# Kernel optimization log

Hardware: AMD Instinct MI355X
Metric: run time of the kernel (lower is better)

The kernel has to match this reference:

```python
import jax, jax.numpy as jnp
import numpy as np

ASPECT = 1.0
SCALE = 0.3
MIN_PATCH_H = 60.0
EPS = 1e-6


def _make_patch_boxes(boxes, H, W):
    # Patcher.create: per detected box, compute [ymin_patch, xmin_patch, patch_h, patch_w]
    ymin, xmin, ymax, xmax = jnp.split(boxes, 4, axis=-1)
    h = ymax - ymin
    w = xmax - xmin
    pw = h * SCALE
    ph = ASPECT * pw
    oy = ymin + h / 2.0
    ox = xmin + w / 2.0
    yp = jnp.maximum(oy - ph / 2.0, 0.0)
    xp = jnp.maximum(ox - pw / 2.0, 0.0)
    yp = jnp.where(yp + ph > H, H - ph, yp)
    xp = jnp.where(xp + pw > W, W - pw, xp)
    return jnp.concatenate([yp, xp, ph, pw], axis=-1)  # [B, N, 4]


def _bilinear(src, rel_y, rel_x, out_h, out_w):
    # tf.image.resize bilinear (half-pixel centers): sample src [P,P,3] at the
    # grid of an (out_h, out_w) resize, evaluated at all H/W image offsets.
    P = src.shape[0]
    sy = jnp.clip((rel_y + 0.5) * P / out_h - 0.5, 0.0, P - 1.0)  # [H]
    sx = jnp.clip((rel_x + 0.5) * P / out_w - 0.5, 0.0, P - 1.0)  # [W]
    y0 = jnp.floor(sy).astype(jnp.int32); y1 = jnp.minimum(y0 + 1, P - 1)
    x0 = jnp.floor(sx).astype(jnp.int32); x1 = jnp.minimum(x0 + 1, P - 1)
    wy = (sy - y0.astype(sy.dtype))[:, None, None]
    wx = (sx - x0.astype(sx.dtype))[None, :, None]
    top = (1.0 - wx) * src[y0[:, None], x0[None, :]] + wx * src[y0[:, None], x1[None, :]]
    bot = (1.0 - wx) * src[y1[:, None], x0[None, :]] + wx * src[y1[:, None], x1[None, :]]
    return (1.0 - wy) * top + wy * bot  # [H, W, 3]


def _forward(images, boxes, patch):
    B, H, W, _ = images.shape
    pboxes = _make_patch_boxes(boxes, float(H), float(W))  # [B, N, 4]
    valid = pboxes[..., 2] > MIN_PATCH_H                    # gather_nd filter
    p_mean = patch.mean((0, 1))
    p_std = patch.std((0, 1)) + EPS
    ys = jnp.arange(H, dtype=jnp.int32)
    xs = jnp.arange(W, dtype=jnp.int32)

    def per_image(image, pbs, vls):
        # serial while_loop over patches: later patches overwrite earlier ones,
        # and histogram match uses the current (already-patched) background.
        def step(img, bv):
            pb, v = bv
            pbi = pb.astype(jnp.int32)  # tf.cast truncation
            y0, x0, ph, pw = pbi[0], pbi[1], pbi[2], pbi[3]
            in_y = (ys >= y0) & (ys < y0 + ph)
            in_x = (xs >= x0) & (xs < x0 + pw)
            mask = in_y[:, None] & in_x[None, :]            # [H, W]
            mf = mask[..., None].astype(img.dtype)
            cnt = jnp.maximum(mask.sum().astype(img.dtype), 1.0)
            bg_mean = (img * mf).sum((0, 1)) / cnt
            bg_std = jnp.sqrt((((img - bg_mean) ** 2) * mf).sum((0, 1)) / cnt) + EPS
            # histogram match (per-channel moment matching) of patch to background
            matched = (patch - p_mean) / p_std * bg_std + bg_mean
            phf = jnp.maximum(ph.astype(img.dtype), 1.0)
            pwf = jnp.maximum(pw.astype(img.dtype), 1.0)
            sampled = _bilinear(matched,
                                (ys - y0).astype(img.dtype),
                                (xs - x0).astype(img.dtype), phf, pwf)
            img = jnp.where(mask[..., None] & v, sampled, img)
            return img, None

        img, _ = jax.lax.scan(step, image, (pbs, vls))
        return img

    return jax.vmap(per_image)(images, pboxes, valid)


def setup_inputs() -> dict:
    key = jax.random.key(0)
    k1, k2, k3 = jax.random.split(key, 3)
    B, N, H, W, P = 16, 16, 512, 512, 512
    images = jax.random.normal(k1, (B, H, W, 3), dtype=jnp.float32)
    u = jax.random.uniform(k2, (B, N, 4), dtype=jnp.float32)
    ymin = u[..., 0] * (H - 320)
    xmin = u[..., 1] * (W - 320)
    h = 150.0 + u[..., 2] * 150.0
    w = 150.0 + u[..., 3] * 150.0
    boxes = jnp.stack([ymin, xmin, ymin + h, xmin + w], axis=-1)
    patch = jax.random.normal(k3, (P, P, 3), dtype=jnp.float32) * 0.5
    return {"images": images, "boxes": boxes, "patch": patch}


def reference(images, boxes, patch):
    return _forward(images, boxes, patch)
```

## Files before the change

kernel.cpp:

```cpp
#include <hip/hip_runtime.h>
#include <math.h>

#define IMG_H 512
#define IMG_W 512
#define PSIZE 512
#define NIMG 16
#define NBOX 16
#define RED_BLOCKS 256
#define Z0 4
#define SLOTS 20

#define WS_PMEAN 0
#define WS_PSTD  3
#define WS_PART  6
#define WS_PAIR  1544
#define WS_COEF  (1544 + 256 * SLOTS * 8)

typedef float f4u __attribute__((ext_vector_type(4), aligned(4)));
typedef float f2u __attribute__((ext_vector_type(2), aligned(4)));

struct BoxGeo { int y0, x0, ph, pw, valid; };

__device__ __forceinline__ BoxGeo make_geo(const float* bx) {
    float ymin = bx[0], xmin = bx[1], ymax = bx[2], xmax = bx[3];
    float h = ymax - ymin, w = xmax - xmin;
    float pwf = h * 0.3f;
    float phf = 1.0f * pwf;
    float oy = ymin + h * 0.5f;
    float ox = xmin + w * 0.5f;
    float yp = fmaxf(oy - phf * 0.5f, 0.0f);
    float xp = fmaxf(ox - pwf * 0.5f, 0.0f);
    if (yp + phf > (float)IMG_H) yp = (float)IMG_H - phf;
    if (xp + pwf > (float)IMG_W) xp = (float)IMG_W - pwf;
    BoxGeo g;
    g.y0 = (int)yp; g.x0 = (int)xp;
    g.ph = (int)phf; g.pw = (int)pwf;
    g.valid = (phf > 60.0f) ? 1 : 0;
    return g;
}

__device__ __forceinline__ void bsample_fast(const float* __restrict__ patch,
                                             int relY, int relX,
                                             float phf, float pwf, float s[3]) {
    float sy = ((float)relY + 0.5f) * (float)PSIZE / phf - 0.5f;
    sy = fminf(fmaxf(sy, 0.0f), (float)(PSIZE - 1));
    float sx = ((float)relX + 0.5f) * (float)PSIZE / pwf - 0.5f;
    sx = fminf(fmaxf(sx, 0.0f), (float)(PSIZE - 1));
    int y0 = (int)floorf(sy);
    int y1 = min(y0 + 1, PSIZE - 1);
    int x0 = (int)floorf(sx);
    float wy = sy - (float)y0;
    float wx = sx - (float)x0;
    const int baseX = min(x0, PSIZE - 2);
    const bool hi = (x0 == PSIZE - 1);
    const float* r0 = patch + (y0 * PSIZE + baseX) * 3;
    const float* r1 = patch + (y1 * PSIZE + baseX) * 3;
    f4u a0 = *(const f4u*)r0; f2u b0 = *(const f2u*)(r0 + 4);
    f4u a1 = *(const f4u*)r1; f2u b1 = *(const f2u*)(r1 + 4);
    float p00c, p01c, p10c, p11c, top, bot;
    p00c = hi ? a0.w : a0.x;  p01c = a0.w;
    p10c = hi ? a1.w : a1.x;  p11c = a1.w;
    top = (1.f - wx) * p00c + wx * p01c;
    bot = (1.f - wx) * p10c + wx * p11c;
    s[0] = (1.f - wy) * top + wy * bot;
    p00c = hi ? b0.x : a0.y;  p01c = b0.x;
    p10c = hi ? b1.x : a1.y;  p11c = b1.x;
    top = (1.f - wx) * p00c + wx * p01c;
    bot = (1.f - wx) * p10c + wx * p11c;
    s[1] = (1.f - wy) * top + wy * bot;
    p00c = hi ? b0.y : a0.z;  p01c = b0.y;
    p10c = hi ? b1.y : a1.z;  p11c = b1.y;
    top = (1.f - wx) * p00c + wx * p01c;
    bot = (1.f - wx) * p10c + wx * p11c;
    s[2] = (1.f - wy) * top + wy * bot;
}

template<int N, int NWAVES>
__device__ __forceinline__ void block_reduceN(float v[N]) {
    __shared__ float lds[NWAVES][N];
    const int lane = threadIdx.x & 63;
    const int wave = threadIdx.x >> 6;
    __syncthreads();
#pragma unroll
    for (int k = 0; k < N; ++k) {
#pragma unroll
        for (int off = 32; off > 0; off >>= 1)
            v[k] += __shfl_down(v[k], off, 64);
    }
    if (lane == 0) {
#pragma unroll
        for (int k = 0; k < N; ++k) lds[wave][k] = v[k];
    }
    __syncthreads();
    if (wave == 0) {
#pragma unroll
        for (int k = 0; k < N; ++k) {
            float x = (lane < NWAVES) ? lds[lane][k] : 0.0f;
#pragma unroll
            for (int off = 32; off > 0; off >>= 1)
                x += __shfl_down(x, off, 64);
            if (lane == 0) lds[0][k] = x;
        }
    }
    __syncthreads();
#pragma unroll
    for (int k = 0; k < N; ++k) v[k] = lds[0][k];
}

__global__ void patch_stats_partial(const float* __restrict__ patch,
                                    float* __restrict__ ws) {
    const int g = blockIdx.x * 256 + threadIdx.x;
    const float4* p4 = (const float4*)patch;
    float4 a = p4[3 * g], b = p4[3 * g + 1], c = p4[3 * g + 2];
    float v[6];
    v[0] = a.x + a.w + b.z + c.y;
    v[1] = a.y + b.x + b.w + c.z;
    v[2] = a.z + b.y + c.x + c.w;
    v[3] = a.x*a.x + a.w*a.w + b.z*b.z + c.y*c.y;
    v[4] = a.y*a.y + b.x*b.x + b.w*b.w + c.z*c.z;
    v[5] = a.z*a.z + b.y*b.y + c.x*c.x + c.w*c.w;
    block_reduceN<6, 4>(v);
    if (threadIdx.x == 0) {
        float* o = ws + WS_PART + blockIdx.x * 6;
#pragma unroll
        for (int k = 0; k < 6; ++k) o[k] = v[k];
    }
}

__global__ void patch_stats_final(float* __restrict__ ws) {
    float v[6];
    const float* p = ws + WS_PART + threadIdx.x * 6;
#pragma unroll
    for (int k = 0; k < 6; ++k) v[k] = p[k];
    block_reduceN<6, 4>(v);
    if (threadIdx.x == 0) {
        const float n = (float)(PSIZE * PSIZE);
#pragma unroll
        for (int c = 0; c < 3; ++c) {
            float m = v[c] / n;
            float var = v[3 + c] / n - m * m;
            ws[WS_PMEAN + c] = m;
            ws[WS_PSTD + c] = sqrtf(fmaxf(var, 0.f)) + 1e-6f;
        }
    }
}

__launch_bounds__(256)
__global__ void pair_sums(const float* __restrict__ images,
                          const float* __restrict__ boxes,
                          const float* __restrict__ patch,
                          float* __restrict__ ws) {
    const int bi = blockIdx.x;
    const int j_idx = blockIdx.y;
    const int z = blockIdx.z;
    const int b = bi >> 4, i = bi & 15;
    if (j_idx > i) return;
    if (j_idx >= 1 && z > 0) return;

    const BoxGeo gi = make_geo(boxes + (b * NBOX + i) * 4);
    if (!gi.valid) return;

    const int slot = (j_idx == 0) ? z : (Z0 + j_idx - 1);
    float* o = ws + WS_PAIR + ((size_t)bi * SLOTS + slot) * 8;

    int ry0 = gi.y0, rx0 = gi.x0;
    int ry1 = gi.y0 + gi.ph, rx1 = gi.x0 + gi.pw;
    int jy0 = 0, jx0 = 0, jph = -1;
    float jphf = 1.f, jpwf = 1.f;
    if (j_idx >= 1) {
        const BoxGeo gj = make_geo(boxes + (b * NBOX + j_idx - 1) * 4);
        if (!gj.valid) {
            if (threadIdx.x == 0) { for (int k = 0; k < 7; ++k) o[k] = 0.f; }
            return;
        }
        ry0 = max(ry0, gj.y0); rx0 = max(rx0, gj.x0);
        ry1 = min(ry1, gj.y0 + gj.ph); rx1 = min(rx1, gj.x0 + gj.pw);
        jy0 = gj.y0; jx0 = gj.x0; jph = gj.ph;
        jphf = (float)gj.ph; jpwf = (float)gj.pw;
    }
    const int rw = rx1 - rx0, rh = ry1 - ry0;
    if (rw <= 0 || rh <= 0) {
        if (threadIdx.x == 0) { for (int k = 0; k < 7; ++k) o[k] = 0.f; }
        return;
    }

    __shared__ BoxGeo geo[NBOX];
    if (threadIdx.x < NBOX)
        geo[threadIdx.x] = make_geo(boxes + (b * NBOX + threadIdx.x) * 4);
    __syncthreads();

    const int n = rw * rh;
    const float* img = images + (size_t)b * IMG_H * IMG_W * 3;
    const int nz = (j_idx == 0) ? Z0 : 1;

    float v[7] = {0.f, 0.f, 0.f, 0.f, 0.f, 0.f, 0.f};
    for (int t = z * 256 + threadIdx.x; t < n; t += 256 * nz) {
        const int y = ry0 + t / rw;
        const int x = rx0 + t % rw;
        bool inc = true;
        for (int k = j_idx; k < i; ++k) {
            const BoxGeo gk = geo[k];
            if (gk.valid && y >= gk.y0 && y < gk.y0 + gk.ph &&
                x >= gk.x0 && x < gk.x0 + gk.pw) { inc = false; break; }
        }
        if (inc) {
            float s[3];
            if (jph > 0) {
                bsample_fast(patch, y - jy0, x - jx0, jphf, jpwf, s);
            } else {
                const float* p = img + ((size_t)y * IMG_W + x) * 3;
                s[0] = p[0]; s[1] = p[1]; s[2] = p[2];
            }
            v[0] += 1.f;
            v[1] += s[0]; v[2] += s[1]; v[3] += s[2];
            v[4] += s[0]*s[0]; v[5] += s[1]*s[1]; v[6] += s[2]*s[2];
        }
    }
    block_reduceN<7, 4>(v);
    if (threadIdx.x == 0) {
#pragma unroll
        for (int k = 0; k < 7; ++k) o[k] = v[k];
    }
}

__global__ void solve_coeffs(const float* __restrict__ boxes,
                             float* __restrict__ ws) {
    const int b = blockIdx.x;
    const int lane = threadIdx.x;

    BoxGeo g = make_geo(boxes + (b * NBOX + (lane < NBOX ? lane : NBOX - 1)) * 4);
    float pm[3], ps[3];
#pragma unroll
    for (int c = 0; c < 3; ++c) { pm[c] = ws[WS_PMEAN + c]; ps[c] = ws[WS_PSTD + c]; }

    float sc[3] = {0.f, 0.f, 0.f}, of[3] = {0.f, 0.f, 0.f};

    for (int i = 0; i < NBOX; ++i) {
        const int valid_i = __shfl(g.valid, i, 64);
        if (!valid_i) continue;

        float cnt = 0.f, s1[3] = {0.f,0.f,0.f}, s2[3] = {0.f,0.f,0.f};
        if (lane <= i) {
            const int slot0 = (lane == 0) ? 0 : (Z0 + lane - 1);
            const int nz = (lane == 0) ? Z0 : 1;
            const float* p = ws + WS_PAIR +
                ((size_t)(b * NBOX + i) * SLOTS + slot0) * 8;
            for (int zz = 0; zz < nz; ++zz) {
                cnt   += p[zz*8 + 0];
                s1[0] += p[zz*8 + 1]; s1[1] += p[zz*8 + 2]; s1[2] += p[zz*8 + 3];
                s2[0] += p[zz*8 + 4]; s2[1] += p[zz*8 + 5]; s2[2] += p[zz*8 + 6];
            }
        }
        float ts[3], tq[3];
#pragma unroll
        for (int c = 0; c < 3; ++c) {
            if (lane == 0) { ts[c] = s1[c]; tq[c] = s2[c]; }
            else {
                ts[c] = sc[c] * s1[c] + of[c] * cnt;
                tq[c] = sc[c]*sc[c]*s2[c] + 2.f*sc[c]*of[c]*s1[c] + of[c]*of[c]*cnt;
            }
        }
#pragma unroll
        for (int c = 0; c < 3; ++c) {
#pragma unroll
            for (int off = 16; off > 0; off >>= 1) {
                ts[c] += __shfl_down(ts[c], off, 32);
                tq[c] += __shfl_down(tq[c], off, 32);
            }
        }
        const int phi = __shfl(g.ph, i, 64);
        const int pwi = __shfl(g.pw, i, 64);
        const float cntf = fmaxf((float)(phi * pwi), 1.0f);
        float nsc[3] = {0.f,0.f,0.f}, nof[3] = {0.f,0.f,0.f};
        if (lane == 0) {
#pragma unroll
            for (int c = 0; c < 3; ++c) {
                float mean = ts[c] / cntf;
                float var = tq[c] / cntf - mean * mean;
                float sd = sqrtf(fmaxf(var, 0.f)) + 1e-6f;
                nsc[c] = sd / ps[c];
                nof[c] = mean - pm[c] * nsc[c];
            }
        }
#pragma unroll
        for (int c = 0; c < 3; ++c) {
            float bs = __shfl(nsc[c], 0, 64);
            float bo = __shfl(nof[c], 0, 64);
            if (lane == i + 1) { sc[c] = bs; of[c] = bo; }
            if (lane == 0) {
                ws[WS_COEF + (size_t)(b * NBOX + i) * 8 + c] = bs;
                ws[WS_COEF + (size_t)(b * NBOX + i) * 8 + 3 + c] = bo;
            }
        }
    }
}

__launch_bounds__(256)
__global__ void render(const float* __restrict__ images,
                       const float* __restrict__ boxes,
                       const float* __restrict__ patch,
                       const float* __restrict__ ws,
                       float* __restrict__ out) {
    const int b = blockIdx.y;
    const int tid = threadIdx.x;
    __shared__ BoxGeo geo[NBOX];
    __shared__ float coef[NBOX][6];
    __shared__ int smask;

    const int strip_y0 = blockIdx.x * 2;

    if (tid == 0) smask = 0;
    if (tid < NBOX)
        geo[tid] = make_geo(boxes + (b * NBOX + tid) * 4);
    if (tid < NBOX * 6) {
        int i = tid / 6, c = tid % 6;
        coef[i][c] = ws[WS_COEF + (size_t)(b * NBOX + i) * 8 + c];
    }
    __syncthreads();
    if (tid < NBOX) {
        const BoxGeo g = geo[tid];
        if (g.valid && g.y0 < strip_y0 + 2 && g.y0 + g.ph > strip_y0)
            atomicOr(&smask, 1 << tid);
    }
    __syncthreads();

    const int q = blockIdx.x * 256 + tid;
    const float4* src = (const float4*)(images + (size_t)b * IMG_H * IMG_W * 3);
    float4* dst = (float4*)(out + (size_t)b * IMG_H * IMG_W * 3);
    const int mask = smask;

    if (mask == 0) {
        dst[3*q]     = src[3*q];
        dst[3*q + 1] = src[3*q + 1];
        dst[3*q + 2] = src[3*q + 2];
        return;
    }

    const int p0 = q << 2;
    const int y = p0 >> 9, x0 = p0 & 511;

    int last[4];
    bool any_un = false;
#pragma unroll
    for (int u = 0; u < 4; ++u) {
        const int x = x0 + u;
        int lj = -1;
        int m = mask;
        while (m) {
            const int j = 31 - __clz(m);
            const BoxGeo g = geo[j];
            if (y >= g.y0 && y < g.y0 + g.ph && x >= g.x0 && x < g.x0 + g.pw) {
                lj = j; break;
            }
            m &= ~(1 << j);
        }
        last[u] = lj;
        any_un |= (lj < 0);
    }

    float4 f[3];
    if (any_un) { f[0] = src[3*q]; f[1] = src[3*q + 1]; f[2] = src[3*q + 2]; }
    float* r = (float*)f;

#pragma unroll
    for (int u = 0; u < 4; ++u) {
        if (last[u] >= 0) {
            const BoxGeo g = geo[last[u]];
            float s[3];
            bsample_fast(patch, y - g.y0, (x0 + u) - g.x0,
                         (float)g.ph, (float)g.pw, s);
            r[3*u + 0] = s[0] * coef[last[u]][0] + coef[last[u]][3];
            r[3*u + 1] = s[1] * coef[last[u]][1] + coef[last[u]][4];
            r[3*u + 2] = s[2] * coef[last[u]][2] + coef[last[u]][5];
        }
    }
    dst[3*q] = f[0]; dst[3*q + 1] = f[1]; dst[3*q + 2] = f[2];
}

extern "C" void kernel_launch(void* const* d_in, const int* in_sizes, int n_in,
                              void* d_out, int out_size, void* d_ws, size_t ws_size,
                              hipStream_t stream) {
    const float* images = (const float*)d_in[0];
    const float* boxes  = (const float*)d_in[1];
    const float* patch  = (const float*)d_in[2];
    float* out = (float*)d_out;
    float* ws  = (float*)d_ws;

    patch_stats_partial<<<RED_BLOCKS, 256, 0, stream>>>(patch, ws);
    patch_stats_final<<<1, RED_BLOCKS, 0, stream>>>(ws);
    pair_sums<<<dim3(NIMG * NBOX, 17, Z0), 256, 0, stream>>>(images, boxes, patch, ws);
    solve_coeffs<<<NIMG, 64, 0, stream>>>(boxes, ws);
    render<<<dim3(IMG_H * IMG_W / 4 / 256, NIMG), 256, 0, stream>>>(images, boxes, patch, ws, out);
}
```

Before: 104.9 us.

## Fuse image copy, stats finalize and pair sums; render decals per box

Merges the patch-stats finalize, the pair-sum reductions and a bulk image-to-output copy into one persistent-style kernel, so the copy overlaps with the reduction work and one launch is saved. The final render no longer re-reads the whole image per pixel. Instead, a per-box decal kernel writes only each box's pixels that no later box covers. Z0 doubles the split of the j=0 reduction. This trades the full-image masked render pass for scattered, non-vectorized 3-float writes inside box regions.

Result: slower. 116.9 us (+11.4%).

```diff
diff --git a/kernel.cpp b/kernel.cpp
--- a/kernel.cpp
+++ b/kernel.cpp
@@ -6,9 +6,12 @@
 #define PSIZE 512
 #define NIMG 16
 #define NBOX 16
-#define RED_BLOCKS 256
-#define Z0 4
-#define SLOTS 20
+#define Z0 8
+#define SLOTS 24
+#define NTASK (256 * 17 * Z0)
+#define NCOPY 2048
+#define CHUNK4 1536
+#define FBLOCKS 4096
 
 #define WS_PMEAN 0
 #define WS_PSTD  3
@@ -57,21 +60,18 @@
     const float* r1 = patch + (y1 * PSIZE + baseX) * 3;
     f4u a0 = *(const f4u*)r0; f2u b0 = *(const f2u*)(r0 + 4);
     f4u a1 = *(const f4u*)r1; f2u b1 = *(const f2u*)(r1 + 4);
-    float p00c, p01c, p10c, p11c, top, bot;
-    p00c = hi ? a0.w : a0.x;  p01c = a0.w;
-    p10c = hi ? a1.w : a1.x;  p11c = a1.w;
-    top = (1.f - wx) * p00c + wx * p01c;
-    bot = (1.f - wx) * p10c + wx * p11c;
+    float p00, p01, p10, p11, top, bot;
+    p00 = hi ? a0.w : a0.x;  p01 = a0.w;
+    p10 = hi ? a1.w : a1.x;  p11 = a1.w;
+    top = (1.f - wx) * p00 + wx * p01; bot = (1.f - wx) * p10 + wx * p11;
     s[0] = (1.f - wy) * top + wy * bot;
-    p00c = hi ? b0.x : a0.y;  p01c = b0.x;
-    p10c = hi ? b1.x : a1.y;  p11c = b1.x;
-    top = (1.f - wx) * p00c + wx * p01c;
-    bot = (1.f - wx) * p10c + wx * p11c;
+    p00 = hi ? b0.x : a0.y;  p01 = b0.x;
+    p10 = hi ? b1.x : a1.y;  p11 = b1.x;
+    top = (1.f - wx) * p00 + wx * p01; bot = (1.f - wx) * p10 + wx * p11;
     s[1] = (1.f - wy) * top + wy * bot;
-    p00c = hi ? b0.y : a0.z;  p01c = b0.y;
-    p10c = hi ? b1.y : a1.z;  p11c = b1.y;
-    top = (1.f - wx) * p00c + wx * p01c;
-    bot = (1.f - wx) * p10c + wx * p11c;
+    p00 = hi ? b0.y : a0.z;  p01 = b0.y;
+    p10 = hi ? b1.y : a1.z;  p11 = b1.y;
+    top = (1.f - wx) * p00 + wx * p01; bot = (1.f - wx) * p10 + wx * p11;
     s[2] = (1.f - wy) * top + wy * bot;
 }
 
@@ -127,99 +127,117 @@
     }
 }
 
-__global__ void patch_stats_final(float* __restrict__ ws) {
-    float v[6];
-    const float* p = ws + WS_PART + threadIdx.x * 6;
-#pragma unroll
-    for (int k = 0; k < 6; ++k) v[k] = p[k];
-    block_reduceN<6, 4>(v);
-    if (threadIdx.x == 0) {
-        const float n = (float)(PSIZE * PSIZE);
-#pragma unroll
-        for (int c = 0; c < 3; ++c) {
-            float m = v[c] / n;
-            float var = v[3 + c] / n - m * m;
-            ws[WS_PMEAN + c] = m;
-            ws[WS_PSTD + c] = sqrtf(fmaxf(var, 0.f)) + 1e-6f;
-        }
-    }
-}
-
 __launch_bounds__(256)
-__global__ void pair_sums(const float* __restrict__ images,
-                          const float* __restrict__ boxes,
-                          const float* __restrict__ patch,
-                          float* __restrict__ ws) {
-    const int bi = blockIdx.x;
-    const int j_idx = blockIdx.y;
-    const int z = blockIdx.z;
-    const int b = bi >> 4, i = bi & 15;
-    if (j_idx > i) return;
-    if (j_idx >= 1 && z > 0) return;
-
-    const BoxGeo gi = make_geo(boxes + (b * NBOX + i) * 4);
-    if (!gi.valid) return;
-
-    const int slot = (j_idx == 0) ? z : (Z0 + j_idx - 1);
-    float* o = ws + WS_PAIR + ((size_t)bi * SLOTS + slot) * 8;
-
-    int ry0 = gi.y0, rx0 = gi.x0;
-    int ry1 = gi.y0 + gi.ph, rx1 = gi.x0 + gi.pw;
-    int jy0 = 0, jx0 = 0, jph = -1;
-    float jphf = 1.f, jpwf = 1.f;
-    if (j_idx >= 1) {
-        const BoxGeo gj = make_geo(boxes + (b * NBOX + j_idx - 1) * 4);
-        if (!gj.valid) {
-            if (threadIdx.x == 0) { for (int k = 0; k < 7; ++k) o[k] = 0.f; }
-            return;
-        }
-        ry0 = max(ry0, gj.y0); rx0 = max(rx0, gj.x0);
-        ry1 = min(ry1, gj.y0 + gj.ph); rx1 = min(rx1, gj.x0 + gj.pw);
-        jy0 = gj.y0; jx0 = gj.x0; jph = gj.ph;
-        jphf = (float)gj.ph; jpwf = (float)gj.pw;
-    }
-    const int rw = rx1 - rx0, rh = ry1 - ry0;
-    if (rw <= 0 || rh <= 0) {
-        if (threadIdx.x == 0) { for (int k = 0; k < 7; ++k) o[k] = 0.f; }
-        return;
-    }
-
+__global__ void fused(const float* __restrict__ images,
+                      const float* __restrict__ boxes,
+                      const float* __restrict__ patch,
+                      float* __restrict__ ws,
+                      float* __restrict__ out) {
+    const int tid = threadIdx.x;
     __shared__ BoxGeo geo[NBOX];
-    if (threadIdx.x < NBOX)
-        geo[threadIdx.x] = make_geo(boxes + (b * NBOX + threadIdx.x) * 4);
-    __syncthreads();
-
-    const int n = rw * rh;
-    const float* img = images + (size_t)b * IMG_H * IMG_W * 3;
-    const int nz = (j_idx == 0) ? Z0 : 1;
-
-    float v[7] = {0.f, 0.f, 0.f, 0.f, 0.f, 0.f, 0.f};
-    for (int t = z * 256 + threadIdx.x; t < n; t += 256 * nz) {
-        const int y = ry0 + t / rw;
-        const int x = rx0 + t % rw;
-        bool inc = true;
-        for (int k = j_idx; k < i; ++k) {
-            const BoxGeo gk = geo[k];
-            if (gk.valid && y >= gk.y0 && y < gk.y0 + gk.ph &&
-                x >= gk.x0 && x < gk.x0 + gk.pw) { inc = false; break; }
-        }
-        if (inc) {
-            float s[3];
-            if (jph > 0) {
-                bsample_fast(patch, y - jy0, x - jx0, jphf, jpwf, s);
+    const int total = NTASK + NCOPY + 1;
+
+    for (int it = blockIdx.x; it < total; it += FBLOCKS) {
+        if (it >= NTASK) {
+            if (it < NTASK + NCOPY) {
+                const int c = it - NTASK;
+                const float4* s4 = (const float4*)images;
+                float4* d4 = (float4*)out;
+                const int base = c * CHUNK4 + tid;
+#pragma unroll
+                for (int u = 0; u < 6; ++u)
+                    d4[base + u * 256] = s4[base + u * 256];
             } else {
-                const float* p = img + ((size_t)y * IMG_W + x) * 3;
-                s[0] = p[0]; s[1] = p[1]; s[2] = p[2];
-            }
-            v[0] += 1.f;
-            v[1] += s[0]; v[2] += s[1]; v[3] += s[2];
-            v[4] += s[0]*s[0]; v[5] += s[1]*s[1]; v[6] += s[2]*s[2];
-        }
-    }
-    block_reduceN<7, 4>(v);
-    if (threadIdx.x == 0) {
-#pragma unroll
-        for (int k = 0; k < 7; ++k) o[k] = v[k];
+                float v[6];
+                const float* p = ws + WS_PART + tid * 6;
+#pragma unroll
+                for (int k = 0; k < 6; ++k) v[k] = p[k];
+                block_reduceN<6, 4>(v);
+                if (tid == 0) {
+                    const float n = (float)(PSIZE * PSIZE);
+#pragma unroll
+                    for (int c = 0; c < 3; ++c) {
+                        float m = v[c] / n;
+                        float var = v[3 + c] / n - m * m;
+                        ws[WS_PMEAN + c] = m;
+                        ws[WS_PSTD + c] = sqrtf(fmaxf(var, 0.f)) + 1e-6f;
+                    }
+                }
+            }
+            continue;
+        }
+        const int z = it / (17 * 256);
+        const int rem = it % (17 * 256);
+        const int j_idx = rem >> 8;
+        const int bi = rem & 255;
+        const int b = bi >> 4, i = bi & 15;
+        if (j_idx > i) continue;
+        if (j_idx >= 1 && z > 0) continue;
+
+        const BoxGeo gi = make_geo(boxes + (b * NBOX + i) * 4);
+        if (!gi.valid) continue;
+
+        const int slot = (j_idx == 0) ? z : (Z0 + j_idx - 1);
+        float* o = ws + WS_PAIR + ((size_t)bi * SLOTS + slot) * 8;
+
+        int ry0 = gi.y0, rx0 = gi.x0;
+        int ry1 = gi.y0 + gi.ph, rx1 = gi.x0 + gi.pw;
+        int jy0 = 0, jx0 = 0, jph = -1;
+        float jphf = 1.f, jpwf = 1.f;
+        if (j_idx >= 1) {
+            const BoxGeo gj = make_geo(boxes + (b * NBOX + j_idx - 1) * 4);
+            if (!gj.valid) {
+                if (tid == 0) { for (int k = 0; k < 7; ++k) o[k] = 0.f; }
+                continue;
+            }
+            ry0 = max(ry0, gj.y0); rx0 = max(rx0, gj.x0);
+            ry1 = min(ry1, gj.y0 + gj.ph); rx1 = min(rx1, gj.x0 + gj.pw);
+            jy0 = gj.y0; jx0 = gj.x0; jph = gj.ph;
+            jphf = (float)gj.ph; jpwf = (float)gj.pw;
+        }
+        const int rw = rx1 - rx0, rh = ry1 - ry0;
+        if (rw <= 0 || rh <= 0) {
+            if (tid == 0) { for (int k = 0; k < 7; ++k) o[k] = 0.f; }
+            continue;
+        }
+
+        __syncthreads();
+        if (tid < NBOX)
+            geo[tid] = make_geo(boxes + (b * NBOX + tid) * 4);
+        __syncthreads();
+
+        const int n = rw * rh;
+        const float* img = images + (size_t)b * IMG_H * IMG_W * 3;
+        const int nz = (j_idx == 0) ? Z0 : 1;
+
+        float v[7] = {0.f, 0.f, 0.f, 0.f, 0.f, 0.f, 0.f};
+        for (int t = z * 256 + tid; t < n; t += 256 * nz) {
+            const int y = ry0 + t / rw;
+            const int x = rx0 + t % rw;
+            bool inc = true;
+            for (int k = j_idx; k < i; ++k) {
+                const BoxGeo gk = geo[k];
+                if (gk.valid && y >= gk.y0 && y < gk.y0 + gk.ph &&
+                    x >= gk.x0 && x < gk.x0 + gk.pw) { inc = false; break; }
+            }
+            if (inc) {
+                float s[3];
+                if (jph > 0) {
+                    bsample_fast(patch, y - jy0, x - jx0, jphf, jpwf, s);
+                } else {
+                    const float* p = img + ((size_t)y * IMG_W + x) * 3;
+                    s[0] = p[0]; s[1] = p[1]; s[2] = p[2];
+                }
+                v[0] += 1.f;
+                v[1] += s[0]; v[2] += s[1]; v[3] += s[2];
+                v[4] += s[0]*s[0]; v[5] += s[1]*s[1]; v[6] += s[2]*s[2];
+            }
+        }
+        block_reduceN<7, 4>(v);
+        if (tid == 0) {
+#pragma unroll
+            for (int k = 0; k < 7; ++k) o[k] = v[k];
+        }
     }
 }
 
@@ -296,85 +314,45 @@
 }
 
 __launch_bounds__(256)
-__global__ void render(const float* __restrict__ images,
-                       const float* __restrict__ boxes,
-                       const float* __restrict__ patch,
-                       const float* __restrict__ ws,
-                       float* __restrict__ out) {
-    const int b = blockIdx.y;
-    const int tid = threadIdx.x;
+__global__ void decal(const float* __restrict__ boxes,
+                      const float* __restrict__ patch,
+                      const float* __restrict__ ws,
+                      float* __restrict__ out) {
+    const int bi = blockIdx.x;
+    const int b = bi >> 4, i = bi & 15;
+    const int z = blockIdx.y;
     __shared__ BoxGeo geo[NBOX];
-    __shared__ float coef[NBOX][6];
-    __shared__ int smask;
-
-    const int strip_y0 = blockIdx.x * 2;
-
-    if (tid == 0) smask = 0;
-    if (tid < NBOX)
-        geo[tid] = make_geo(boxes + (b * NBOX + tid) * 4);
-    if (tid < NBOX * 6) {
-        int i = tid / 6, c = tid % 6;
-        coef[i][c] = ws[WS_COEF + (size_t)(b * NBOX + i) * 8 + c];
-    }
+    __shared__ float coef[6];
+    if (threadIdx.x < NBOX)
+        geo[threadIdx.x] = make_geo(boxes + (b * NBOX + threadIdx.x) * 4);
+    if (threadIdx.x >= 32 && threadIdx.x < 38)
+        coef[threadIdx.x - 32] = ws[WS_COEF + (size_t)bi * 8 + (threadIdx.x - 32)];
     __syncthreads();
-    if (tid < NBOX) {
-        const BoxGeo g = geo[tid];
-        if (g.valid && g.y0 < strip_y0 + 2 && g.y0 + g.ph > strip_y0)
-            atomicOr(&smask, 1 << tid);
-    }
-    __syncthreads();
-
-    const int q = blockIdx.x * 256 + tid;
-    const float4* src = (const float4*)(images + (size_t)b * IMG_H * IMG_W * 3);
-    float4* dst = (float4*)(out + (size_t)b * IMG_H * IMG_W * 3);
-    const int mask = smask;
-
-    if (mask == 0) {
-        dst[3*q]     = src[3*q];
-        dst[3*q + 1] = src[3*q + 1];
-        dst[3*q + 2] = src[3*q + 2];
-        return;
-    }
-
-    const int p0 = q << 2;
-    const int y = p0 >> 9, x0 = p0 & 511;
-
-    int last[4];
-    bool any_un = false;
-#pragma unroll
-    for (int u = 0; u < 4; ++u) {
-        const int x = x0 + u;
-        int lj = -1;
-        int m = mask;
-        while (m) {
-            const int j = 31 - __clz(m);
-            const BoxGeo g = geo[j];
-            if (y >= g.y0 && y < g.y0 + g.ph && x >= g.x0 && x < g.x0 + g.pw) {
-                lj = j; break;
-            }
-            m &= ~(1 << j);
-        }
-        last[u] = lj;
-        any_un |= (lj < 0);
-    }
-
-    float4 f[3];
-    if (any_un) { f[0] = src[3*q]; f[1] = src[3*q + 1]; f[2] = src[3*q + 2]; }
-    float* r = (float*)f;
-
-#pragma unroll
-    for (int u = 0; u < 4; ++u) {
-        if (last[u] >= 0) {
-            const BoxGeo g = geo[last[u]];
+    const BoxGeo gi = geo[i];
+    if (!gi.valid) return;
+    const int y0 = gi.y0, x0 = gi.x0, ph = gi.ph, pw = gi.pw;
+    const int n = ph * pw;
+    const float phf = (float)ph, pwf = (float)pw;
+    float* img = out + (size_t)b * IMG_H * IMG_W * 3;
+
+    for (int t = z * 256 + threadIdx.x; t < n; t += 256 * 8) {
+        const int y = y0 + t / pw;
+        const int x = x0 + t % pw;
+        bool cov = false;
+        for (int k = i + 1; k < NBOX; ++k) {
+            const BoxGeo g = geo[k];
+            if (g.valid && y >= g.y0 && y < g.y0 + g.ph &&
+                x >= g.x0 && x < g.x0 + g.pw) { cov = true; break; }
+        }
+        if (!cov) {
             float s[3];
-            bsample_fast(patch, y - g.y0, (x0 + u) - g.x0,
-                         (float)g.ph, (float)g.pw, s);
-            r[3*u + 0] = s[0] * coef[last[u]][0] + coef[last[u]][3];
-            r[3*u + 1] = s[1] * coef[last[u]][1] + coef[last[u]][4];
-            r[3*u + 2] = s[2] * coef[last[u]][2] + coef[last[u]][5];
-        }
-    }
-    dst[3*q] = f[0]; dst[3*q + 1] = f[1]; dst[3*q + 2] = f[2];
+            bsample_fast(patch, y - y0, x - x0, phf, pwf, s);
+            float* o = img + ((size_t)y * IMG_W + x) * 3;
+            o[0] = s[0] * coef[0] + coef[3];
+            o[1] = s[1] * coef[1] + coef[4];
+            o[2] = s[2] * coef[2] + coef[5];
+        }
+    }
 }
 
 extern "C" void kernel_launch(void* const* d_in, const int* in_sizes, int n_in,
@@ -386,9 +364,8 @@
     float* out = (float*)d_out;
     float* ws  = (float*)d_ws;
 
-    patch_stats_partial<<<RED_BLOCKS, 256, 0, stream>>>(patch, ws);
-    patch_stats_final<<<1, RED_BLOCKS, 0, stream>>>(ws);
-    pair_sums<<<dim3(NIMG * NBOX, 17, Z0), 256, 0, stream>>>(images, boxes, patch, ws);
+    patch_stats_partial<<<256, 256, 0, stream>>>(patch, ws);
+    fused<<<FBLOCKS, 256, 0, stream>>>(images, boxes, patch, ws, out);
     solve_coeffs<<<NIMG, 64, 0, stream>>>(boxes, ws);
-    render<<<dim3(IMG_H * IMG_W / 4 / 256, NIMG), 256, 0, stream>>>(images, boxes, patch, ws, out);
-}
+    decal<<<dim3(NIMG * NBOX, 8), 256, 0, stream>>>(boxes, patch, ws, out);
+}
```
